# Optimization experiments

Hardware: AMD Instinct MI355X
Metric: run time of the kernel (lower is better)

The kernel has to match this reference:

```python
import jax, jax.numpy as jnp
import numpy as np

T, D, H, E = 8192, 1024, 2048, 8


def setup_inputs() -> dict:
    key = jax.random.key(0)
    k1, k2, k3 = jax.random.split(key, 3)
    x = jax.random.normal(k1, (T, D), dtype=jnp.float32)
    # counts must sum to T; use a uniform split (reference handles any valid split)
    num_tokens_per_expert = jnp.full((E,), T // E, dtype=jnp.int32)
    w_up = jax.random.normal(k2, (E, H, D), dtype=jnp.float32) * (1.0 / np.sqrt(D))
    w_down = jax.random.normal(k3, (E, D, H), dtype=jnp.float32) * (1.0 / np.sqrt(H))
    return {"x": x, "num_tokens_per_expert": num_tokens_per_expert, "w_up": w_up, "w_down": w_down}


def reference(x, num_tokens_per_expert, w_up, w_down):
    """Grouped MoE expert MLP: per-expert  x @ w_up[e].T -> relu^2 -> @ w_down[e].T.
    Tokens are sorted by expert; counts encode the segment boundaries.
    Matches the CUDA path: bf16 compute for both GEMMs and the activation,
    final cast back to x.dtype.
    """
    n_tok = x.shape[0]
    n_exp = w_up.shape[0]
    # segment id per token from cumulative offsets (same as grouped_mm offs)
    offsets = jnp.cumsum(num_tokens_per_expert)  # (E,)
    expert_id = jnp.searchsorted(offsets, jnp.arange(n_tok), side="right")  # (T,)

    xb = x.astype(jnp.bfloat16)
    wu = w_up.astype(jnp.bfloat16)   # (E, H, D)
    wd = w_down.astype(jnp.bfloat16)  # (E, D, H)

    out = jnp.zeros((n_tok, x.shape[1]), dtype=jnp.bfloat16)
    # small fixed loop over experts; token dim fully vectorized
    for e in range(n_exp):
        h = jnp.maximum(xb @ wu[e].T, 0)          # (T, H) relu
        h = (h * h).astype(jnp.bfloat16)           # square, re-cast as original
        y = h @ wd[e].T                            # (T, D)
        out = out + jnp.where((expert_id == e)[:, None], y, jnp.bfloat16(0))
    return out.astype(x.dtype)
```

## Files before the change

### kernel.cpp

```cpp
#include <hip/hip_runtime.h>
#include <stdint.h>

constexpr int T_TOK = 8192;
constexpr int D_DIM = 1024;
constexpr int H_DIM = 2048;
constexpr int E_NUM = 8;

typedef __bf16 bf16x8 __attribute__((ext_vector_type(8)));
typedef float  f32x4  __attribute__((ext_vector_type(4)));

static __device__ __forceinline__ unsigned short f2bf(float f) {
  union { float f; unsigned u; } a; a.f = f;
  unsigned r = a.u + 0x7fffu + ((a.u >> 16) & 1u);
  return (unsigned short)(r >> 16);
}

__global__ void cvt_f32_bf16(const float* __restrict__ src,
                             unsigned short* __restrict__ dst, int n4) {
  int i = blockIdx.x * blockDim.x + threadIdx.x;
  int stride = gridDim.x * blockDim.x;
  for (; i < n4; i += stride) {
    float4 v = reinterpret_cast<const float4*>(src)[i];
    ushort4 o;
    o.x = f2bf(v.x); o.y = f2bf(v.y); o.z = f2bf(v.z); o.w = f2bf(v.w);
    reinterpret_cast<ushort4*>(dst)[i] = o;
  }
}

#define FENCE() asm volatile("" ::: "memory")
#define BARRIER() do { FENCE(); __builtin_amdgcn_s_barrier(); FENCE(); } while (0)
#define WAIT_LGKM0() asm volatile("s_waitcnt lgkmcnt(0)" ::: "memory")
#define WAIT_VM(N) asm volatile("s_waitcnt vmcnt(%0)" :: "i"(N) : "memory")

template <int K_DIM, int N_DIM, int BN, bool RELU2>
__global__ __launch_bounds__(512, 2)
void ggt(const unsigned short* __restrict__ A,
         const float* __restrict__ Bw,
         const int* __restrict__ counts,
         void* __restrict__ Cout) {
  constexpr int BM = 256, BK = 32;
  constexpr int NT = K_DIM / BK;
  constexpr int WN = BN / 4;
  constexpr int NACC = WN / 16;
  constexpr int BI  = BN / 64;
  constexpr int ISS = 2 + BI;

  const int tid  = threadIdx.x;
  const int wid  = tid >> 6;
  const int lane = tid & 63;
  const int wr   = wid >> 2;
  const int wc   = wid & 3;

  const int id = blockIdx.x + gridDim.x * blockIdx.y;
  const int ct = id & 7;
  const int rt = id >> 3;

  int t = rt;
  int e = -1, rowBase = 0, rowsValid = 0;
  {
    int tiles = 0, off = 0;
#pragma unroll
    for (int i = 0; i < E_NUM; ++i) {
      int n  = counts[i];
      int nt = (n + BM - 1) / BM;
      if (e < 0 && t < tiles + nt) {
        e = i;
        int lt = t - tiles;
        rowBase   = off + lt * BM;
        rowsValid = n - lt * BM;
        if (rowsValid > BM) rowsValid = BM;
      }
      tiles += nt; off += n;
    }
  }
  if (e < 0) return;
  const int colBase = ct * BN;

  __shared__ __align__(1024) char lds[3 * (BM * 64 + BN * 128)];
  auto ldsA = [&](int b) -> char* { return lds + b * (BM * 64); };
  auto ldsB = [&](int b) -> char* { return lds + 3 * (BM * 64) + b * (BN * 128); };

  const char* gA = (const char*)A + (size_t)rowBase * (K_DIM * 2);
  const char* gB = (const char*)Bw + ((size_t)e * N_DIM + colBase) * (size_t)(K_DIM * 4);

  auto stageA = [&](int buf, int kt) {
#pragma unroll
    for (int j = 0; j < 2; ++j) {
      int row0u = j * 128 + wid * 16;
      int r  = row0u + (lane >> 2);
      int sr = (r < rowsValid) ? r : rowsValid - 1;
      int sg = (lane & 3) ^ ((r >> 1) & 3);
      const char* src = gA + (size_t)sr * (K_DIM * 2) + (size_t)kt * 64 + sg * 16;
      __builtin_amdgcn_global_load_lds(
          (const __attribute__((address_space(1))) void*)src,
          (__attribute__((address_space(3))) void*)(ldsA(buf) + row0u * 64),
          16, 0, 0);
    }
  };
  auto stageB = [&](int buf, int kt) {
#pragma unroll
    for (int j = 0; j < BI; ++j) {
      int row0u = j * 64 + wid * 8;
      int r  = row0u + (lane >> 3);
      int sg = (lane & 7) ^ (r & 7);
      const char* src = gB + (size_t)r * (K_DIM * 4) + (size_t)kt * 128 + sg * 16;
      __builtin_amdgcn_global_load_lds(
          (const __attribute__((address_space(1))) void*)src,
          (__attribute__((address_space(3))) void*)(ldsB(buf) + row0u * 128),
          16, 0, 0);
    }
  };

  const int rl = lane & 15;
  const int gh = lane >> 4;

  bf16x8 aF[8], bF[NACC];
  f32x4  accC[8][NACC];
#pragma unroll
  for (int m = 0; m < 8; ++m)
#pragma unroll
    for (int n = 0; n < NACC; ++n) accC[m][n] = (f32x4){0.f, 0.f, 0.f, 0.f};

  auto readA = [&](int buf) {
    const char* base = ldsA(buf);
#pragma unroll
    for (int m = 0; m < 8; ++m) {
      int r = wr * 128 + m * 16 + rl;
      int g = gh ^ ((r >> 1) & 3);
      aF[m] = *(const bf16x8*)(base + r * 64 + g * 16);
    }
  };
  auto readB = [&](int buf) {
    const char* base = ldsB(buf);
#pragma unroll
    for (int n = 0; n < NACC; ++n) {
      int r = wc * WN + n * 16 + rl;
      const char* rb = base + r * 128;
      f32x4 v0 = *(const f32x4*)(rb + (((2 * gh + 0) ^ (r & 7)) * 16));
      f32x4 v1 = *(const f32x4*)(rb + (((2 * gh + 1) ^ (r & 7)) * 16));
      union { __bf16 b[8]; bf16x8 v; } u;
#pragma unroll
      for (int p = 0; p < 4; ++p) {
        u.b[p]     = (__bf16)v0[p];
        u.b[4 + p] = (__bf16)v1[p];
      }
      bF[n] = u.v;
    }
  };

  stageA(0, 0); stageB(0, 0);
  stageA(1, 1); stageB(1, 1);

  for (int t2 = 0; t2 < NT; ++t2) {
    WAIT_VM(ISS);
    BARRIER();
    const int ks = (t2 + 2 < NT) ? t2 + 2 : NT - 1;
    const int bs = (t2 + 2) % 3;
    const int bc = t2 % 3;
    stageA(bs, ks);
    stageB(bs, ks);
    readA(bc);
    readB(bc);
    WAIT_LGKM0();
    __builtin_amdgcn_s_setprio(1);
#pragma unroll
    for (int m = 0; m < 8; ++m)
#pragma unroll
      for (int n = 0; n < NACC; ++n)
        accC[m][n] = __builtin_amdgcn_mfma_f32_16x16x32_bf16(
            aF[m], bF[n], accC[m][n], 0, 0, 0);
    __builtin_amdgcn_s_setprio(0);
  }
  WAIT_VM(0);

  const int rB0 = wr * 128 + gh * 4;
  const int cB0 = colBase + wc * WN + rl;
#pragma unroll
  for (int m = 0; m < 8; ++m) {
#pragma unroll
    for (int n = 0; n < NACC; ++n) {
#pragma unroll
      for (int j = 0; j < 4; ++j) {
        int r = rB0 + m * 16 + j;
        if (r < rowsValid) {
          size_t idx = (size_t)(rowBase + r) * N_DIM + (cB0 + n * 16);
          float v = accC[m][n][j];
          if (RELU2) {
            float rv = v > 0.f ? v : 0.f;
            float hf = (float)(__bf16)rv;
            ((__bf16*)Cout)[idx] = (__bf16)(hf * hf);
          } else {
            ((float*)Cout)[idx] = (float)(__bf16)v;
          }
        }
      }
    }
  }
}

extern "C" void kernel_launch(void* const* d_in, const int* in_sizes, int n_in,
                              void* d_out, int out_size, void* d_ws, size_t ws_size,
                              hipStream_t stream) {
  const float* x   = (const float*)d_in[0];
  const int*   cnt = (const int*)d_in[1];
  const float* wu  = (const float*)d_in[2];
  const float* wd  = (const float*)d_in[3];
  float* out = (float*)d_out;
  char*  ws  = (char*)d_ws;

  unsigned short* xb   = (unsigned short*)(ws);
  unsigned short* hbuf = (unsigned short*)(ws + (16u << 20));

  cvt_f32_bf16<<<2048, 256, 0, stream>>>(x, xb, T_TOK * D_DIM / 4);

  ggt<D_DIM, H_DIM, 256, true ><<<dim3(40, H_DIM / 256), dim3(512), 0, stream>>>(
      xb, wu, cnt, (void*)hbuf);
  ggt<H_DIM, D_DIM, 128, false><<<dim3(40, D_DIM / 128), dim3(512), 0, stream>>>(
      hbuf, wd, cnt, (void*)out);
}
```

Before: 112.4 us.

## Fuse x fp32-to-bf16 conversion into first grouped GEMM, drop convert kernel

Removes the standalone x conversion kernel and adds a dedicated up-projection kernel that loads fp32 x tiles straight into LDS and converts them to bf16 on the fragment read, as was already done for the weights. This drops one launch plus a 32MB read and 16MB write of the bf16 copy. In exchange, A-tile traffic doubles per K step and LDS grows. The pipeline also goes from triple to double buffering with a full vmcnt(0) wait each step, so load latency is exposed more and memory/compute overlap is lower.

```diff
diff --git a/kernel.cpp b/kernel.cpp
--- a/kernel.cpp
+++ b/kernel.cpp
@@ -9,28 +9,155 @@
 typedef __bf16 bf16x8 __attribute__((ext_vector_type(8)));
 typedef float  f32x4  __attribute__((ext_vector_type(4)));
 
-static __device__ __forceinline__ unsigned short f2bf(float f) {
-  union { float f; unsigned u; } a; a.f = f;
-  unsigned r = a.u + 0x7fffu + ((a.u >> 16) & 1u);
-  return (unsigned short)(r >> 16);
-}
-
-__global__ void cvt_f32_bf16(const float* __restrict__ src,
-                             unsigned short* __restrict__ dst, int n4) {
-  int i = blockIdx.x * blockDim.x + threadIdx.x;
-  int stride = gridDim.x * blockDim.x;
-  for (; i < n4; i += stride) {
-    float4 v = reinterpret_cast<const float4*>(src)[i];
-    ushort4 o;
-    o.x = f2bf(v.x); o.y = f2bf(v.y); o.z = f2bf(v.z); o.w = f2bf(v.w);
-    reinterpret_cast<ushort4*>(dst)[i] = o;
-  }
-}
-
 #define FENCE() asm volatile("" ::: "memory")
 #define BARRIER() do { FENCE(); __builtin_amdgcn_s_barrier(); FENCE(); } while (0)
 #define WAIT_LGKM0() asm volatile("s_waitcnt lgkmcnt(0)" ::: "memory")
 #define WAIT_VM(N) asm volatile("s_waitcnt vmcnt(%0)" :: "i"(N) : "memory")
+
+__global__ __launch_bounds__(512, 2)
+void ggx(const float* __restrict__ X,
+         const float* __restrict__ Bw,
+         const int* __restrict__ counts,
+         unsigned short* __restrict__ Hout) {
+  constexpr int K_DIM = D_DIM, N_DIM = H_DIM;
+  constexpr int BM = 256, BK = 32, BN = 256;
+  constexpr int NT = K_DIM / BK;
+  constexpr int WN = 64, NACC = 4;
+
+  const int tid  = threadIdx.x;
+  const int wid  = tid >> 6;
+  const int lane = tid & 63;
+  const int wr   = wid >> 2;
+  const int wc   = wid & 3;
+
+  const int id = blockIdx.x + gridDim.x * blockIdx.y;
+  const int ct = id & 7;
+  const int rt = id >> 3;
+
+  int t = rt;
+  int e = -1, rowBase = 0, rowsValid = 0;
+  {
+    int tiles = 0, off = 0;
+#pragma unroll
+    for (int i = 0; i < E_NUM; ++i) {
+      int n  = counts[i];
+      int nt = (n + BM - 1) / BM;
+      if (e < 0 && t < tiles + nt) {
+        e = i;
+        int lt = t - tiles;
+        rowBase   = off + lt * BM;
+        rowsValid = n - lt * BM;
+        if (rowsValid > BM) rowsValid = BM;
+      }
+      tiles += nt; off += n;
+    }
+  }
+  if (e < 0) return;
+  const int colBase = ct * BN;
+
+  __shared__ __align__(1024) char lds[4 * BM * 128];
+  auto ldsA = [&](int b) -> char* { return lds + b * (BM * 128); };
+  auto ldsB = [&](int b) -> char* { return lds + (2 + b) * (BM * 128); };
+
+  const char* gA = (const char*)X + (size_t)rowBase * (K_DIM * 4);
+  const char* gB = (const char*)Bw + ((size_t)e * N_DIM + colBase) * (size_t)(K_DIM * 4);
+
+  auto stageA = [&](int buf, int kt) {
+#pragma unroll
+    for (int j = 0; j < 4; ++j) {
+      int row0u = j * 64 + wid * 8;
+      int r  = row0u + (lane >> 3);
+      int sr = (r < rowsValid) ? r : rowsValid - 1;
+      int sg = (lane & 7) ^ (r & 7);
+      const char* src = gA + (size_t)sr * (K_DIM * 4) + (size_t)kt * 128 + sg * 16;
+      __builtin_amdgcn_global_load_lds(
+          (const __attribute__((address_space(1))) void*)src,
+          (__attribute__((address_space(3))) void*)(ldsA(buf) + row0u * 128),
+          16, 0, 0);
+    }
+  };
+  auto stageB = [&](int buf, int kt) {
+#pragma unroll
+    for (int j = 0; j < 4; ++j) {
+      int row0u = j * 64 + wid * 8;
+      int r  = row0u + (lane >> 3);
+      int sg = (lane & 7) ^ (r & 7);
+      const char* src = gB + (size_t)r * (K_DIM * 4) + (size_t)kt * 128 + sg * 16;
+      __builtin_amdgcn_global_load_lds(
+          (const __attribute__((address_space(1))) void*)src,
+          (__attribute__((address_space(3))) void*)(ldsB(buf) + row0u * 128),
+          16, 0, 0);
+    }
+  };
+
+  const int rl = lane & 15;
+  const int gh = lane >> 4;
+
+  bf16x8 aF[8], bF[NACC];
+  f32x4  accC[8][NACC];
+#pragma unroll
+  for (int m = 0; m < 8; ++m)
+#pragma unroll
+    for (int n = 0; n < NACC; ++n) accC[m][n] = (f32x4){0.f, 0.f, 0.f, 0.f};
+
+  auto readF = [&](const char* base, int r) -> bf16x8 {
+    const char* rb = base + r * 128;
+    f32x4 v0 = *(const f32x4*)(rb + (((2 * gh + 0) ^ (r & 7)) * 16));
+    f32x4 v1 = *(const f32x4*)(rb + (((2 * gh + 1) ^ (r & 7)) * 16));
+    union { __bf16 b[8]; bf16x8 v; } u;
+#pragma unroll
+    for (int p = 0; p < 4; ++p) {
+      u.b[p]     = (__bf16)v0[p];
+      u.b[4 + p] = (__bf16)v1[p];
+    }
+    return u.v;
+  };
+
+  stageA(0, 0); stageB(0, 0);
+
+  for (int t2 = 0; t2 < NT; ++t2) {
+    WAIT_VM(0);
+    BARRIER();
+    const int ks = (t2 + 1 < NT) ? t2 + 1 : NT - 1;
+    const int bn = (t2 + 1) & 1, bc = t2 & 1;
+    stageA(bn, ks);
+    stageB(bn, ks);
+#pragma unroll
+    for (int m = 0; m < 8; ++m) aF[m] = readF(ldsA(bc), wr * 128 + m * 16 + rl);
+#pragma unroll
+    for (int n = 0; n < NACC; ++n) bF[n] = readF(ldsB(bc), wc * WN + n * 16 + rl);
+    WAIT_LGKM0();
+    __builtin_amdgcn_s_setprio(1);
+#pragma unroll
+    for (int m = 0; m < 8; ++m)
+#pragma unroll
+      for (int n = 0; n < NACC; ++n)
+        accC[m][n] = __builtin_amdgcn_mfma_f32_16x16x32_bf16(
+            aF[m], bF[n], accC[m][n], 0, 0, 0);
+    __builtin_amdgcn_s_setprio(0);
+  }
+  WAIT_VM(0);
+
+  const int rB0 = wr * 128 + gh * 4;
+  const int cB0 = colBase + wc * WN + rl;
+#pragma unroll
+  for (int m = 0; m < 8; ++m) {
+#pragma unroll
+    for (int n = 0; n < NACC; ++n) {
+#pragma unroll
+      for (int j = 0; j < 4; ++j) {
+        int r = rB0 + m * 16 + j;
+        if (r < rowsValid) {
+          size_t idx = (size_t)(rowBase + r) * N_DIM + (cB0 + n * 16);
+          float v = accC[m][n][j];
+          float rv = v > 0.f ? v : 0.f;
+          float hf = (float)(__bf16)rv;
+          ((__bf16*)Hout)[idx] = (__bf16)(hf * hf);
+        }
+      }
+    }
+  }
+}
 
 template <int K_DIM, int N_DIM, int BN, bool RELU2>
 __global__ __launch_bounds__(512, 2)
@@ -208,13 +335,10 @@
   float* out = (float*)d_out;
   char*  ws  = (char*)d_ws;
 
-  unsigned short* xb   = (unsigned short*)(ws);
-  unsigned short* hbuf = (unsigned short*)(ws + (16u << 20));
-
-  cvt_f32_bf16<<<2048, 256, 0, stream>>>(x, xb, T_TOK * D_DIM / 4);
-
-  ggt<D_DIM, H_DIM, 256, true ><<<dim3(40, H_DIM / 256), dim3(512), 0, stream>>>(
-      xb, wu, cnt, (void*)hbuf);
+  unsigned short* hbuf = (unsigned short*)(ws);
+
+  ggx<<<dim3(40, H_DIM / 256), dim3(512), 0, stream>>>(x, wu, cnt, hbuf);
+
   ggt<H_DIM, D_DIM, 128, false><<<dim3(40, D_DIM / 128), dim3(512), 0, stream>>>(
       hbuf, wd, cnt, (void*)out);
 }
```

Result: slower. 115.1 us (+2.4%).

## Replace large 256-row tiles with 128x128 tiles, 4 waves, double buffering

Applied to the files above, without the earlier changes.

Reworks both grouped GEMMs to use 128x128 output tiles with 256-thread blocks (4 waves, 2x2) in place of 256xBN tiles with 512 threads. The LDS pipeline drops from triple to double buffering, with a full vmcnt wait each iteration. The grid grows to 72 row tiles to cover the smaller tiles, which raises block count and occupancy for better CU fill. In exchange, each MFMA does less reuse per loaded byte, fp32 weights are reloaded more often, and the shallower prefetch exposes more memory latency.

```diff
diff --git a/kernel.cpp b/kernel.cpp
--- a/kernel.cpp
+++ b/kernel.cpp
@@ -32,28 +32,26 @@
 #define WAIT_LGKM0() asm volatile("s_waitcnt lgkmcnt(0)" ::: "memory")
 #define WAIT_VM(N) asm volatile("s_waitcnt vmcnt(%0)" :: "i"(N) : "memory")
 
-template <int K_DIM, int N_DIM, int BN, bool RELU2>
-__global__ __launch_bounds__(512, 2)
-void ggt(const unsigned short* __restrict__ A,
-         const float* __restrict__ Bw,
-         const int* __restrict__ counts,
-         void* __restrict__ Cout) {
-  constexpr int BM = 256, BK = 32;
+template <int K_DIM, int N_DIM, bool RELU2>
+__global__ __launch_bounds__(256, 4)
+void gg128(const unsigned short* __restrict__ A,
+           const float* __restrict__ Bw,
+           const int* __restrict__ counts,
+           void* __restrict__ Cout) {
+  constexpr int BM = 128, BK = 32, BN = 128;
   constexpr int NT = K_DIM / BK;
-  constexpr int WN = BN / 4;
-  constexpr int NACC = WN / 16;
-  constexpr int BI  = BN / 64;
-  constexpr int ISS = 2 + BI;
+  constexpr int NCOLT = N_DIM / BN;
 
   const int tid  = threadIdx.x;
   const int wid  = tid >> 6;
   const int lane = tid & 63;
-  const int wr   = wid >> 2;
-  const int wc   = wid & 3;
+  const int wr   = wid >> 1;
+  const int wc   = wid & 1;
 
   const int id = blockIdx.x + gridDim.x * blockIdx.y;
-  const int ct = id & 7;
-  const int rt = id >> 3;
+  int ct, rt;
+  if constexpr (NCOLT == 16) { ct = (id & 7) | (((id >> 3) & 1) << 3); rt = id >> 4; }
+  else                       { ct = id & 7;                            rt = id >> 3; }
 
   int t = rt;
   int e = -1, rowBase = 0, rowsValid = 0;
@@ -76,9 +74,9 @@
   if (e < 0) return;
   const int colBase = ct * BN;
 
-  __shared__ __align__(1024) char lds[3 * (BM * 64 + BN * 128)];
+  __shared__ __align__(1024) char lds[2 * (BM * 64) + 2 * (BN * 128)];
   auto ldsA = [&](int b) -> char* { return lds + b * (BM * 64); };
-  auto ldsB = [&](int b) -> char* { return lds + 3 * (BM * 64) + b * (BN * 128); };
+  auto ldsB = [&](int b) -> char* { return lds + 2 * (BM * 64) + b * (BN * 128); };
 
   const char* gA = (const char*)A + (size_t)rowBase * (K_DIM * 2);
   const char* gB = (const char*)Bw + ((size_t)e * N_DIM + colBase) * (size_t)(K_DIM * 4);
@@ -86,7 +84,7 @@
   auto stageA = [&](int buf, int kt) {
 #pragma unroll
     for (int j = 0; j < 2; ++j) {
-      int row0u = j * 128 + wid * 16;
+      int row0u = j * 64 + wid * 16;
       int r  = row0u + (lane >> 2);
       int sr = (r < rowsValid) ? r : rowsValid - 1;
       int sg = (lane & 3) ^ ((r >> 1) & 3);
@@ -99,8 +97,8 @@
   };
   auto stageB = [&](int buf, int kt) {
 #pragma unroll
-    for (int j = 0; j < BI; ++j) {
-      int row0u = j * 64 + wid * 8;
+    for (int j = 0; j < 4; ++j) {
+      int row0u = j * 32 + wid * 8;
       int r  = row0u + (lane >> 3);
       int sg = (lane & 7) ^ (r & 7);
       const char* src = gB + (size_t)r * (K_DIM * 4) + (size_t)kt * 128 + sg * 16;
@@ -114,18 +112,18 @@
   const int rl = lane & 15;
   const int gh = lane >> 4;
 
-  bf16x8 aF[8], bF[NACC];
-  f32x4  accC[8][NACC];
-#pragma unroll
-  for (int m = 0; m < 8; ++m)
-#pragma unroll
-    for (int n = 0; n < NACC; ++n) accC[m][n] = (f32x4){0.f, 0.f, 0.f, 0.f};
+  bf16x8 aF[4], bF[4];
+  f32x4  accC[4][4];
+#pragma unroll
+  for (int m = 0; m < 4; ++m)
+#pragma unroll
+    for (int n = 0; n < 4; ++n) accC[m][n] = (f32x4){0.f, 0.f, 0.f, 0.f};
 
   auto readA = [&](int buf) {
     const char* base = ldsA(buf);
 #pragma unroll
-    for (int m = 0; m < 8; ++m) {
-      int r = wr * 128 + m * 16 + rl;
+    for (int m = 0; m < 4; ++m) {
+      int r = wr * 64 + m * 16 + rl;
       int g = gh ^ ((r >> 1) & 3);
       aF[m] = *(const bf16x8*)(base + r * 64 + g * 16);
     }
@@ -133,8 +131,8 @@
   auto readB = [&](int buf) {
     const char* base = ldsB(buf);
 #pragma unroll
-    for (int n = 0; n < NACC; ++n) {
-      int r = wc * WN + n * 16 + rl;
+    for (int n = 0; n < 4; ++n) {
+      int r = wc * 64 + n * 16 + rl;
       const char* rb = base + r * 128;
       f32x4 v0 = *(const f32x4*)(rb + (((2 * gh + 0) ^ (r & 7)) * 16));
       f32x4 v1 = *(const f32x4*)(rb + (((2 * gh + 1) ^ (r & 7)) * 16));
@@ -149,36 +147,34 @@
   };
 
   stageA(0, 0); stageB(0, 0);
-  stageA(1, 1); stageB(1, 1);
 
   for (int t2 = 0; t2 < NT; ++t2) {
-    WAIT_VM(ISS);
+    WAIT_VM(0);
     BARRIER();
-    const int ks = (t2 + 2 < NT) ? t2 + 2 : NT - 1;
-    const int bs = (t2 + 2) % 3;
-    const int bc = t2 % 3;
-    stageA(bs, ks);
-    stageB(bs, ks);
+    const int ks = (t2 + 1 < NT) ? t2 + 1 : NT - 1;
+    const int bn = (t2 + 1) & 1, bc = t2 & 1;
+    stageA(bn, ks);
+    stageB(bn, ks);
     readA(bc);
     readB(bc);
     WAIT_LGKM0();
     __builtin_amdgcn_s_setprio(1);
 #pragma unroll
-    for (int m = 0; m < 8; ++m)
-#pragma unroll
-      for (int n = 0; n < NACC; ++n)
+    for (int m = 0; m < 4; ++m)
+#pragma unroll
+      for (int n = 0; n < 4; ++n)
         accC[m][n] = __builtin_amdgcn_mfma_f32_16x16x32_bf16(
             aF[m], bF[n], accC[m][n], 0, 0, 0);
     __builtin_amdgcn_s_setprio(0);
   }
   WAIT_VM(0);
 
-  const int rB0 = wr * 128 + gh * 4;
-  const int cB0 = colBase + wc * WN + rl;
-#pragma unroll
-  for (int m = 0; m < 8; ++m) {
-#pragma unroll
-    for (int n = 0; n < NACC; ++n) {
+  const int rB0 = wr * 64 + gh * 4;
+  const int cB0 = colBase + wc * 64 + rl;
+#pragma unroll
+  for (int m = 0; m < 4; ++m) {
+#pragma unroll
+    for (int n = 0; n < 4; ++n) {
 #pragma unroll
       for (int j = 0; j < 4; ++j) {
         int r = rB0 + m * 16 + j;
@@ -213,8 +209,8 @@
 
   cvt_f32_bf16<<<2048, 256, 0, stream>>>(x, xb, T_TOK * D_DIM / 4);
 
-  ggt<D_DIM, H_DIM, 256, true ><<<dim3(40, H_DIM / 256), dim3(512), 0, stream>>>(
+  gg128<D_DIM, H_DIM, true ><<<dim3(72, H_DIM / 128), dim3(256), 0, stream>>>(
       xb, wu, cnt, (void*)hbuf);
-  ggt<H_DIM, D_DIM, 128, false><<<dim3(40, D_DIM / 128), dim3(512), 0, stream>>>(
+  gg128<H_DIM, D_DIM, false><<<dim3(72, D_DIM / 128), dim3(256), 0, stream>>>(
       hbuf, wd, cnt, (void*)out);
 }
```

After: 132.6 us. 18.0% more time.
